# Kernel tuning notes

Measured on AMD Instinct MI355X. Metric: run time of the kernel, lower is better.

The kernel has to match this reference:

```python
import jax, jax.numpy as jnp
import numpy as np

N_HEADS = 2


def _ln(x, g, b, eps=1e-5):
    m = x.mean(-1, keepdims=True)
    v = ((x - m) ** 2).mean(-1, keepdims=True)
    return (x - m) * jax.lax.rsqrt(v + eps) * g + b


def _mha(x, in_w, in_b, out_w, out_b):
    # standard multi-head self-attention (relative/rotary branch is inert: query_pos=None)
    B, S, d = x.shape
    hd = d // N_HEADS
    qkv = x @ in_w.T + in_b
    q, k, v = jnp.split(qkv, 3, axis=-1)
    q = q.reshape(B, S, N_HEADS, hd)
    k = k.reshape(B, S, N_HEADS, hd)
    v = v.reshape(B, S, N_HEADS, hd)
    scores = jnp.einsum('bqhd,bkhd->bhqk', q, k) / jnp.sqrt(jnp.asarray(hd, x.dtype))
    attn = jax.nn.softmax(scores, axis=-1)
    o = jnp.einsum('bhqk,bkhd->bqhd', attn, v).reshape(B, S, d)
    return o @ out_w.T + out_b


def _forward(x, w1, b1, attn_in_w, attn_in_b, attn_out_w, attn_out_b, ln1_g, ln1_b,
             ffw_w1, ffw_b1, ffw_w2, ffw_b2, ln2_g, ln2_b,
             in_proj_w, conv_w, conv_b, x_proj_w, dt_proj_w, dt_proj_b, A_log, D, out_proj_w,
             w2a, b2a, w2b, b2b, w3a, b3a, w3b, b3b):
    # mlp1: (B,S,1) -> (B,S,d)
    h = x @ w1.T + b1
    # FFWRelativeSelfAttentionModule: 2 layers of post-norm MHA + FFW, take last output
    for i in range(2):
        a = _mha(h, attn_in_w[i], attn_in_b[i], attn_out_w[i], attn_out_b[i])
        h = _ln(h + a, ln1_g[i], ln1_b[i])
        f = jax.nn.relu(h @ ffw_w1[i].T + ffw_b1[i]) @ ffw_w2[i].T + ffw_b2[i]
        h = _ln(h + f, ln2_g[i], ln2_b[i])
    # Mamba block
    xz = h @ in_proj_w.T                       # (B,S,2*di)
    xm, z = jnp.split(xz, 2, axis=-1)          # (B,S,di) each
    S_len = xm.shape[1]
    dcv = conv_w.shape[1]
    xp = jnp.pad(xm, ((0, 0), (dcv - 1, 0), (0, 0)))   # causal depthwise conv1d
    xc = conv_b + sum(conv_w[:, k] * xp[:, k:k + S_len, :] for k in range(dcv))
    xc = jax.nn.silu(xc)
    xdb = xc @ x_proj_w.T                      # (B,S,dt_rank+2*N)
    dt_r = dt_proj_w.shape[1]
    N = A_log.shape[1]
    dti = xdb[..., :dt_r]
    Bm = xdb[..., dt_r:dt_r + N]
    Cm = xdb[..., dt_r + N:]
    dt = jax.nn.softplus(dti @ dt_proj_w.T + dt_proj_b)   # (B,S,di)
    A = -jnp.exp(A_log)                                    # (di,N)

    def step(hst, inp):
        dt_t, B_t, C_t, x_t = inp              # (B,di),(B,N),(B,N),(B,di)
        hst = hst * jnp.exp(dt_t[..., None] * A) + dt_t[..., None] * B_t[:, None, :] * x_t[..., None]
        y = jnp.einsum('bdn,bn->bd', hst, C_t)
        return hst, y

    h0 = jnp.zeros((xc.shape[0], A.shape[0], N), xc.dtype)
    xs = (jnp.swapaxes(dt, 0, 1), jnp.swapaxes(Bm, 0, 1),
          jnp.swapaxes(Cm, 0, 1), jnp.swapaxes(xc, 0, 1))
    _, ys = jax.lax.scan(step, h0, xs)
    y = jnp.swapaxes(ys, 0, 1) + D * xc
    y = y * jax.nn.silu(z)
    h = y @ out_proj_w.T                       # (B,S,d)
    # mlp2 (two stacked Linears, no activation) -> (B,S,1)
    o = (h @ w2a.T + b2a) @ w2b.T + b2b
    o = o.reshape(o.shape[0], -1)              # (B,9)
    # mlp3
    o = jax.nn.relu(o @ w3a.T + b3a) @ w3b.T + b3b
    return o


def setup_inputs() -> dict:
    key = jax.random.key(0)
    ks = jax.random.split(key, 16)
    d, N, dcv, di, dtr, B, S = 256, 16, 4, 512, 16, 4096, 9
    rn = lambda k, shp, s=0.02: jax.random.normal(k, shp, jnp.float32) * s
    return {
        'x': jax.random.normal(ks[0], (B, S, 1), jnp.float32),
        'w1': rn(ks[1], (d, 1), 0.5), 'b1': jnp.zeros((d,)),
        'attn_in_w': rn(ks[2], (2, 3 * d, d)), 'attn_in_b': jnp.zeros((2, 3 * d)),
        'attn_out_w': rn(ks[3], (2, d, d)), 'attn_out_b': jnp.zeros((2, d)),
        'ln1_g': jnp.ones((2, d)), 'ln1_b': jnp.zeros((2, d)),
        'ffw_w1': rn(ks[4], (2, d, d)), 'ffw_b1': jnp.zeros((2, d)),
        'ffw_w2': rn(ks[5], (2, d, d)), 'ffw_b2': jnp.zeros((2, d)),
        'ln2_g': jnp.ones((2, d)), 'ln2_b': jnp.zeros((2, d)),
        'in_proj_w': rn(ks[6], (2 * di, d)),
        'conv_w': rn(ks[7], (di, dcv), 0.2), 'conv_b': jnp.zeros((di,)),
        'x_proj_w': rn(ks[8], (dtr + 2 * N, di)),
        'dt_proj_w': rn(ks[9], (di, dtr), 0.1), 'dt_proj_b': jnp.full((di,), -4.0),
        'A_log': jnp.log(jnp.broadcast_to(jnp.arange(1, N + 1, dtype=jnp.float32), (di, N))),
        'D': jnp.ones((di,)),
        'out_proj_w': rn(ks[10], (d, di)),
        'w2a': rn(ks[11], (32, d)), 'b2a': jnp.zeros((32,)),
        'w2b': rn(ks[12], (1, 32)), 'b2b': jnp.zeros((1,)),
        'w3a': rn(ks[13], (9, 9), 0.3), 'b3a': jnp.zeros((9,)),
        'w3b': rn(ks[14], (1, 9), 0.3), 'b3b': jnp.zeros((1,)),
    }


def reference(x, w1, b1, attn_in_w, attn_in_b, attn_out_w, attn_out_b, ln1_g, ln1_b,
              ffw_w1, ffw_b1, ffw_w2, ffw_b2, ln2_g, ln2_b,
              in_proj_w, conv_w, conv_b, x_proj_w, dt_proj_w, dt_proj_b, A_log, D, out_proj_w,
              w2a, b2a, w2b, b2b, w3a, b3a, w3b, b3b):
    return _forward(x, w1, b1, attn_in_w, attn_in_b, attn_out_w, attn_out_b, ln1_g, ln1_b,
                    ffw_w1, ffw_b1, ffw_w2, ffw_b2, ln2_g, ln2_b,
                    in_proj_w, conv_w, conv_b, x_proj_w, dt_proj_w, dt_proj_b, A_log, D, out_proj_w,
                    w2a, b2a, w2b, b2b, w3a, b3a, w3b, b3b)
```

## Files before the change

### kernel.cpp

```cpp
#include <hip/hip_runtime.h>
#include <hip/hip_bf16.h>
#include <math.h>


#define BATCH 4096

typedef __attribute__((ext_vector_type(8))) short short8;
typedef __attribute__((ext_vector_type(4))) float f32x4;
typedef __attribute__((ext_vector_type(4))) unsigned short u16x4;
typedef unsigned short ushort;

__device__ __forceinline__ ushort f2bf(float f) {
    unsigned u = __float_as_uint(f);
    u += 0x7fffu + ((u >> 16) & 1u);
    return (ushort)(u >> 16);
}
__device__ __forceinline__ float bf2f(ushort u) {
    return __uint_as_float(((unsigned)u) << 16);
}

__global__ __launch_bounds__(256) void convw_kernel(
    const float* __restrict__ s0, const float* __restrict__ s1,
    const float* __restrict__ s2, const float* __restrict__ s3,
    const float* __restrict__ s4, const float* __restrict__ s5,
    ushort* __restrict__ dst)
{
    int i = blockIdx.x * 256 + threadIdx.x;
    float v;
    if      (i < 393216)  v = s0[i];
    else if (i < 524288)  v = s1[i - 393216];
    else if (i < 655360)  v = s2[i - 524288];
    else if (i < 786432)  v = s3[i - 655360];
    else if (i < 1048576) v = s4[i - 786432];
    else                  v = s5[i - 1048576];
    dst[i] = f2bf(v);
}

__global__ __launch_bounds__(256) void embed_kernel(
    const float* __restrict__ x, const float* __restrict__ w1,
    const float* __restrict__ b1, float* __restrict__ h,
    ushort* __restrict__ hbf, int r0, int nr)
{
    int i = blockIdx.x * 256 + threadIdx.x;
    if (i >= nr * 256) return;
    int c  = i & 255;
    int row = i >> 8;
    float v = x[r0 + row] * w1[c] + b1[c];
    h[i] = v;
    hbf[i] = f2bf(v);
}

__global__ __launch_bounds__(256) void mgemm_kernel(
    const ushort* __restrict__ A, const ushort* __restrict__ W,
    const float* __restrict__ bias, float* __restrict__ Cf,
    ushort* __restrict__ Cb, const float* __restrict__ yin,
    int M, int N, int K, int lda, int act, int outmode)
{
    __shared__ ushort As[128 * 64];
    __shared__ ushort Bs[128 * 64];

    const int tid  = threadIdx.x;
    const int m0   = blockIdx.x * 128;
    const int n0   = blockIdx.y * 128;
    const int wid  = tid >> 6, lane = tid & 63;
    const int wr   = wid >> 1, wc = wid & 1;
    const int lrow = lane & 15, lk8 = lane >> 4, l7 = lane & 7;
    const int trow = tid >> 3, tchk = tid & 7;

    f32x4 acc[4][4];
    #pragma unroll
    for (int i = 0; i < 4; ++i)
        #pragma unroll
        for (int j = 0; j < 4; ++j)
            acc[i][j] = f32x4{0.f, 0.f, 0.f, 0.f};

    for (int k0 = 0; k0 < K; k0 += 64) {
        #pragma unroll
        for (int p = 0; p < 4; ++p) {
            const int r = p * 32 + trow;
            const short8 av = *reinterpret_cast<const short8*>(
                &A[(size_t)(m0 + r) * lda + k0 + tchk * 8]);
            const short8 wv = *reinterpret_cast<const short8*>(
                &W[(size_t)(n0 + r) * K + k0 + tchk * 8]);
            const int off = r * 64 + ((tchk ^ (r & 7)) << 3);
            *reinterpret_cast<short8*>(&As[off]) = av;
            *reinterpret_cast<short8*>(&Bs[off]) = wv;
        }
        __syncthreads();

        #pragma unroll
        for (int kh = 0; kh < 2; ++kh) {
            short8 af[4], bf[4];
            #pragma unroll
            for (int i = 0; i < 4; ++i) {
                const int ra = wr * 64 + i * 16 + lrow;
                const int rb = wc * 64 + i * 16 + lrow;
                const int sl = ((kh << 2) | lk8) ^ l7;
                af[i] = *reinterpret_cast<const short8*>(&As[ra * 64 + sl * 8]);
                bf[i] = *reinterpret_cast<const short8*>(&Bs[rb * 64 + sl * 8]);
            }
            #pragma unroll
            for (int i = 0; i < 4; ++i)
                #pragma unroll
                for (int j = 0; j < 4; ++j)
                    acc[i][j] = __builtin_amdgcn_mfma_f32_16x16x32_bf16(
                        af[i], bf[j], acc[i][j], 0, 0, 0);
        }
        __syncthreads();
    }

    const int cb = n0 + wc * 64 + lrow;
    const int rb = m0 + wr * 64 + lk8 * 4;
    float bj[4];
    #pragma unroll
    for (int j = 0; j < 4; ++j) bj[j] = bias ? bias[cb + j * 16] : 0.f;

    #pragma unroll
    for (int i = 0; i < 4; ++i) {
        #pragma unroll
        for (int r = 0; r < 4; ++r) {
            const size_t mrow = (size_t)(rb + i * 16 + r) * N;
            #pragma unroll
            for (int j = 0; j < 4; ++j) {
                float v = acc[i][j][r] + bj[j];
                const size_t idx = mrow + cb + j * 16;
                if (act == 1) v = fmaxf(v, 0.f);
                if (outmode == 0) {
                    Cf[idx] = v;
                } else if (outmode == 1) {
                    Cb[idx] = f2bf(v);
                } else {
                    const float sig = 1.f / (1.f + __expf(-v));
                    Cb[idx] = f2bf(yin[idx] * (v * sig));
                }
            }
        }
    }
}

__global__ __launch_bounds__(256) void sgemm_kernel(
    const float* __restrict__ A, const float* __restrict__ W,
    const float* __restrict__ bias, float* __restrict__ C,
    int M, int N, int K, int lda, int act)
{
    __shared__ float As[16][68];
    __shared__ float Ws[16][68];
    const int tid = threadIdx.x;
    const int m0 = blockIdx.y * 64;
    const int n0 = blockIdx.x * 64;
    const int tm = tid >> 4;
    const int tn = tid & 15;
    const int lrow = tid >> 2;
    const int lk   = (tid & 3) * 4;

    float acc[4][4] = {};

    for (int k0 = 0; k0 < K; k0 += 16) {
        {
            int m = m0 + lrow;
            float4 v = make_float4(0.f, 0.f, 0.f, 0.f);
            if (m < M) v = *reinterpret_cast<const float4*>(&A[(size_t)m * lda + k0 + lk]);
            As[lk + 0][lrow] = v.x; As[lk + 1][lrow] = v.y;
            As[lk + 2][lrow] = v.z; As[lk + 3][lrow] = v.w;
            int n = n0 + lrow;
            float4 w = make_float4(0.f, 0.f, 0.f, 0.f);
            if (n < N) w = *reinterpret_cast<const float4*>(&W[(size_t)n * K + k0 + lk]);
            Ws[lk + 0][lrow] = w.x; Ws[lk + 1][lrow] = w.y;
            Ws[lk + 2][lrow] = w.z; Ws[lk + 3][lrow] = w.w;
        }
        __syncthreads();
        #pragma unroll
        for (int k = 0; k < 16; ++k) {
            float4 av = *reinterpret_cast<const float4*>(&As[k][tm * 4]);
            float4 wv = *reinterpret_cast<const float4*>(&Ws[k][tn * 4]);
            float a[4] = {av.x, av.y, av.z, av.w};
            float w[4] = {wv.x, wv.y, wv.z, wv.w};
            #pragma unroll
            for (int i = 0; i < 4; ++i)
                #pragma unroll
                for (int j = 0; j < 4; ++j)
                    acc[i][j] = fmaf(a[i], w[j], acc[i][j]);
        }
        __syncthreads();
    }

    #pragma unroll
    for (int i = 0; i < 4; ++i) {
        int m = m0 + tm * 4 + i;
        if (m >= M) continue;
        #pragma unroll
        for (int j = 0; j < 4; ++j) {
            int n = n0 + tn * 4 + j;
            if (n >= N) continue;
            float v = acc[i][j];
            if (bias) v += bias[n];
            if (act == 1) v = fmaxf(v, 0.f);
            C[(size_t)m * N + n] = v;
        }
    }
}

__global__ __launch_bounds__(128) void attn_kernel(
    const ushort* __restrict__ qkv, ushort* __restrict__ o, int nb)
{
    __shared__ float q[9][132], kk[9][132], v[9][132];
    __shared__ float sc[9][12];
    const int blk = blockIdx.x;
    if (blk >= nb * 2) return;
    const int b = blk >> 1, head = blk & 1;
    const int t = threadIdx.x;
    const size_t base = (size_t)b * 9 * 768 + (size_t)head * 128;
    #pragma unroll
    for (int s = 0; s < 9; ++s) {
        q[s][t]  = bf2f(qkv[base + s * 768 + t]);
        kk[s][t] = bf2f(qkv[base + s * 768 + 256 + t]);
        v[s][t]  = bf2f(qkv[base + s * 768 + 512 + t]);
    }
    __syncthreads();
    if (t < 81) {
        int qi = t / 9, ki = t % 9;
        float acc = 0.f;
        #pragma unroll 8
        for (int c = 0; c < 128; ++c) acc = fmaf(q[qi][c], kk[ki][c], acc);
        sc[qi][ki] = acc * 0.08838834764831845f;
    }
    __syncthreads();
    if (t < 9) {
        float mx = -1e30f;
        #pragma unroll
        for (int k2 = 0; k2 < 9; ++k2) mx = fmaxf(mx, sc[t][k2]);
        float e[9], sum = 0.f;
        #pragma unroll
        for (int k2 = 0; k2 < 9; ++k2) { e[k2] = __expf(sc[t][k2] - mx); sum += e[k2]; }
        float inv = 1.f / sum;
        #pragma unroll
        for (int k2 = 0; k2 < 9; ++k2) sc[t][k2] = e[k2] * inv;
    }
    __syncthreads();
    #pragma unroll
    for (int qi = 0; qi < 9; ++qi) {
        float acc = 0.f;
        #pragma unroll
        for (int k2 = 0; k2 < 9; ++k2) acc = fmaf(sc[qi][k2], v[k2][t], acc);
        o[(size_t)(b * 9 + qi) * 256 + head * 128 + t] = f2bf(acc);
    }
}

__global__ __launch_bounds__(256) void ln_add_kernel(
    const float* __restrict__ h, const float* __restrict__ a,
    const float* __restrict__ g, const float* __restrict__ bb,
    float* __restrict__ out, ushort* __restrict__ outbf, int nrows)
{
    const int wave = threadIdx.x >> 6;
    const int lane = threadIdx.x & 63;
    const int row = blockIdx.x * 4 + wave;
    if (row >= nrows) return;
    const float4 hv = reinterpret_cast<const float4*>(h + (size_t)row * 256)[lane];
    const float4 av = reinterpret_cast<const float4*>(a + (size_t)row * 256)[lane];
    float x0 = hv.x + av.x, x1 = hv.y + av.y, x2 = hv.z + av.z, x3 = hv.w + av.w;
    float s  = x0 + x1 + x2 + x3;
    float sq = x0 * x0 + x1 * x1 + x2 * x2 + x3 * x3;
    #pragma unroll
    for (int off = 32; off; off >>= 1) {
        s  += __shfl_down(s, off);
        sq += __shfl_down(sq, off);
    }
    s = __shfl(s, 0); sq = __shfl(sq, 0);
    const float mean = s * (1.f / 256.f);
    const float var  = sq * (1.f / 256.f) - mean * mean;
    const float inv  = rsqrtf(var + 1e-5f);
    const float4 gv = reinterpret_cast<const float4*>(g)[lane];
    const float4 bv = reinterpret_cast<const float4*>(bb)[lane];
    float4 ov;
    ov.x = (x0 - mean) * inv * gv.x + bv.x;
    ov.y = (x1 - mean) * inv * gv.y + bv.y;
    ov.z = (x2 - mean) * inv * gv.z + bv.z;
    ov.w = (x3 - mean) * inv * gv.w + bv.w;
    reinterpret_cast<float4*>(out + (size_t)row * 256)[lane] = ov;
    u16x4 bf;
    bf.x = f2bf(ov.x); bf.y = f2bf(ov.y); bf.z = f2bf(ov.z); bf.w = f2bf(ov.w);
    reinterpret_cast<u16x4*>(outbf + (size_t)row * 256)[lane] = bf;
}

__global__ __launch_bounds__(256) void conv_silu2_kernel(
    const float* __restrict__ xm, const float* __restrict__ cw,
    const float* __restrict__ cb, float* __restrict__ xc, int nb)
{
    int i = blockIdx.x * 256 + threadIdx.x;
    if (i >= nb * 512) return;
    const int c = i & 511, b = i >> 9;
    float xmv[9];
    #pragma unroll
    for (int s = 0; s < 9; ++s)
        xmv[s] = xm[(size_t)(b * 9 + s) * 512 + c];
    const float4 cwv4 = *reinterpret_cast<const float4*>(&cw[c * 4]);
    const float cwv[4] = {cwv4.x, cwv4.y, cwv4.z, cwv4.w};
    const float cbv = cb[c];
    #pragma unroll
    for (int s = 0; s < 9; ++s) {
        float acc = cbv;
        #pragma unroll
        for (int k = 0; k < 4; ++k) {
            const int sp = s + k - 3;
            if (sp >= 0) acc = fmaf(cwv[k], xmv[sp], acc);
        }
        const float sig = 1.f / (1.f + __expf(-acc));
        xc[(size_t)(b * 9 + s) * 512 + c] = acc * sig;
    }
}

__global__ __launch_bounds__(512) void scan_kernel(
    float* __restrict__ xcy, const float* __restrict__ xdb,
    const float* __restrict__ dt_w, const float* __restrict__ dt_b,
    const float* __restrict__ A_log, const float* __restrict__ Dp)
{
    __shared__ float sx[9 * 48];
    const int c = threadIdx.x;
    const int b = blockIdx.x;
    if (c < 108) {
        reinterpret_cast<float4*>(sx)[c] =
            reinterpret_cast<const float4*>(xdb + (size_t)b * 432)[c];
    }

    float wdt[16], Ar[16];
    #pragma unroll
    for (int n = 0; n < 16; n += 4) {
        const float4 wv4 = *reinterpret_cast<const float4*>(&dt_w[c * 16 + n]);
        wdt[n] = wv4.x; wdt[n + 1] = wv4.y; wdt[n + 2] = wv4.z; wdt[n + 3] = wv4.w;
        const float4 av4 = *reinterpret_cast<const float4*>(&A_log[c * 16 + n]);
        Ar[n] = -__expf(av4.x); Ar[n + 1] = -__expf(av4.y);
        Ar[n + 2] = -__expf(av4.z); Ar[n + 3] = -__expf(av4.w);
    }
    const float dtb = dt_b[c];
    const float Dc  = Dp[c];
    const float a1  = Ar[0];
    bool chain = true;
    #pragma unroll
    for (int n = 1; n < 16; ++n)
        chain = chain && (fabsf(Ar[n] - (float)(n + 1) * a1) <=
                          1e-3f * (float)(n + 1) * fabsf(a1));
    __syncthreads();

    float hst[16] = {};
    for (int s = 0; s < 9; ++s) {
        const float* xb = sx + s * 48;
        float dti = dtb;
        #pragma unroll
        for (int n = 0; n < 16; ++n) dti = fmaf(xb[n], wdt[n], dti);
        const float dt = (dti > 20.f) ? dti : __logf(1.f + __expf(dti));
        const size_t idx = (size_t)(b * 9 + s) * 512 + c;
        const float xv = xcy[idx];
        const float dtx = dt * xv;
        float acc = 0.f;
        if (chain) {
            const float e1 = __expf(dt * a1);
            float en = 1.f;
            #pragma unroll
            for (int n = 0; n < 16; ++n) {
                en *= e1;
                hst[n] = fmaf(hst[n], en, dtx * xb[16 + n]);
                acc = fmaf(hst[n], xb[32 + n], acc);
            }
        } else {
            #pragma unroll
            for (int n = 0; n < 16; ++n) {
                hst[n] = fmaf(hst[n], __expf(dt * Ar[n]), dtx * xb[16 + n]);
                acc = fmaf(hst[n], xb[32 + n], acc);
            }
        }
        xcy[idx] = acc + Dc * xv;
    }
}

__global__ __launch_bounds__(256) void head_kernel(
    const float* __restrict__ t32, const float* __restrict__ w2b,
    const float* __restrict__ b2b, const float* __restrict__ w3a,
    const float* __restrict__ b3a, const float* __restrict__ w3b,
    const float* __restrict__ b3b, float* __restrict__ out, int b0, int nb)
{
    int b = blockIdx.x * 256 + threadIdx.x;
    if (b >= nb) return;
    float o9[9];
    #pragma unroll
    for (int s = 0; s < 9; ++s) {
        const float* r = t32 + (size_t)(b * 9 + s) * 32;
        float acc = b2b[0];
        #pragma unroll
        for (int k = 0; k < 32; ++k) acc = fmaf(r[k], w2b[k], acc);
        o9[s] = acc;
    }
    float accout = b3b[0];
    #pragma unroll
    for (int j = 0; j < 9; ++j) {
        float rj = b3a[j];
        #pragma unroll
        for (int s = 0; s < 9; ++s) rj = fmaf(o9[s], w3a[j * 9 + s], rj);
        rj = fmaxf(rj, 0.f);
        accout = fmaf(rj, w3b[j], accout);
    }
    out[b0 + b] = accout;
}

extern "C" void kernel_launch(void* const* d_in, const int* in_sizes, int n_in,
                              void* d_out, int out_size, void* d_ws, size_t ws_size,
                              hipStream_t stream)
{
    const float* x          = (const float*)d_in[0];
    const float* w1         = (const float*)d_in[1];
    const float* b1         = (const float*)d_in[2];
    const float* attn_in_w  = (const float*)d_in[3];
    const float* attn_in_b  = (const float*)d_in[4];
    const float* attn_out_w = (const float*)d_in[5];
    const float* attn_out_b = (const float*)d_in[6];
    const float* ln1_g      = (const float*)d_in[7];
    const float* ln1_b      = (const float*)d_in[8];
    const float* ffw_w1     = (const float*)d_in[9];
    const float* ffw_b1     = (const float*)d_in[10];
    const float* ffw_w2     = (const float*)d_in[11];
    const float* ffw_b2     = (const float*)d_in[12];
    const float* ln2_g      = (const float*)d_in[13];
    const float* ln2_b      = (const float*)d_in[14];
    const float* in_proj_w  = (const float*)d_in[15];
    const float* conv_w     = (const float*)d_in[16];
    const float* conv_b     = (const float*)d_in[17];
    const float* x_proj_w   = (const float*)d_in[18];
    const float* dt_proj_w  = (const float*)d_in[19];
    const float* dt_proj_b  = (const float*)d_in[20];
    const float* A_log      = (const float*)d_in[21];
    const float* Dp         = (const float*)d_in[22];
    const float* out_proj_w = (const float*)d_in[23];
    const float* w2a        = (const float*)d_in[24];
    const float* b2a        = (const float*)d_in[25];
    const float* w2b        = (const float*)d_in[26];
    const float* b2b        = (const float*)d_in[27];
    const float* w3a        = (const float*)d_in[28];
    const float* b3a        = (const float*)d_in[29];
    const float* w3b        = (const float*)d_in[30];
    const float* b3b        = (const float*)d_in[31];
    float* out = (float*)d_out;

    const size_t WB_FLOATS = 589824;
    const size_t PER_ROW = 1792;
    int nchunks = 1;
    while (nchunks < 32 &&
           (WB_FLOATS + (size_t)(BATCH / nchunks) * 9 * PER_ROW) * sizeof(float) > ws_size)
        nchunks <<= 1;
    const int nb = BATCH / nchunks;
    const int nr = nb * 9;
    const size_t CAPR = (size_t)nr;

    ushort* WB = (ushort*)d_ws;
    float*  AR = (float*)d_ws + WB_FLOATS;

    ushort* wb_attn_in  = WB;
    ushort* wb_attn_out = WB + 393216;
    ushort* wb_ffw1     = WB + 524288;
    ushort* wb_ffw2     = WB + 655360;
    ushort* wb_inproj_x = WB + 786432;
    ushort* wb_inproj_z = WB + 917504;
    ushort* wb_outproj  = WB + 1048576;

    hipLaunchKernelGGL(convw_kernel, dim3(1179648 / 256), dim3(256), 0, stream,
                       attn_in_w, attn_out_w, ffw_w1, ffw_w2, in_proj_w,
                       out_proj_w, WB);

    auto gemm = [&](const float* A, const float* W, const float* bias, float* C,
                    int M, int N, int K, int lda, int act) {
        dim3 grid((N + 63) / 64, (M + 63) / 64);
        hipLaunchKernelGGL(sgemm_kernel, grid, dim3(256), 0, stream,
                           A, W, bias, C, M, N, K, lda, act);
    };
    auto mgemm = [&](const ushort* A, const ushort* W, const float* bias,
                     float* Cf, ushort* Cb, const float* yin,
                     int M, int N, int K, int lda, int act, int outmode) {
        dim3 grid(M / 128, N / 128);
        hipLaunchKernelGGL(mgemm_kernel, grid, dim3(256), 0, stream,
                           A, W, bias, Cf, Cb, yin, M, N, K, lda, act, outmode);
    };

    for (int ck = 0; ck < nchunks; ++ck) {
        const int b0 = ck * nb;
        const int r0 = b0 * 9;

        float*  h    = AR;
        ushort* hbf  = (ushort*)(AR + CAPR * 256);
        float*  aux  = AR + CAPR * 384;
        ushort* aobf = (ushort*)aux;
        float*  big  = AR + CAPR * 512;
        ushort* qkvb = (ushort*)big;
        float*  aa   = big;
        ushort* f1bf = (ushort*)(big + CAPR * 256);
        float*  f2   = big + CAPR * 384;
        float*  xm   = big;
        ushort* ybf  = (ushort*)(big + CAPR * 512);
        float*  xc   = AR + CAPR * 1280;
        float*  xdb  = aux;
        float*  h2   = h;
        float*  t32  = aux;

        hipLaunchKernelGGL(embed_kernel, dim3((nr * 256 + 255) / 256), dim3(256),
                           0, stream, x, w1, b1, h, hbf, r0, nr);

        for (int i = 0; i < 2; ++i) {
            mgemm(hbf, wb_attn_in + (size_t)i * 196608, attn_in_b + i * 768,
                  nullptr, qkvb, nullptr, nr, 768, 256, 256, 0, 1);
            hipLaunchKernelGGL(attn_kernel, dim3(nb * 2), dim3(128), 0, stream,
                               qkvb, aobf, nb);
            mgemm(aobf, wb_attn_out + (size_t)i * 65536, attn_out_b + i * 256,
                  aa, nullptr, nullptr, nr, 256, 256, 256, 0, 0);
            hipLaunchKernelGGL(ln_add_kernel, dim3((nr + 3) / 4), dim3(256), 0, stream,
                               h, aa, ln1_g + i * 256, ln1_b + i * 256, h, hbf, nr);
            mgemm(hbf, wb_ffw1 + (size_t)i * 65536, ffw_b1 + i * 256,
                  nullptr, f1bf, nullptr, nr, 256, 256, 256, 1, 1);
            mgemm(f1bf, wb_ffw2 + (size_t)i * 65536, ffw_b2 + i * 256,
                  f2, nullptr, nullptr, nr, 256, 256, 256, 0, 0);
            hipLaunchKernelGGL(ln_add_kernel, dim3((nr + 3) / 4), dim3(256), 0, stream,
                               h, f2, ln2_g + i * 256, ln2_b + i * 256, h, hbf, nr);
        }

        mgemm(hbf, wb_inproj_x, nullptr, xm, nullptr, nullptr,
              nr, 512, 256, 256, 0, 0);
        hipLaunchKernelGGL(conv_silu2_kernel, dim3((nb * 512 + 255) / 256), dim3(256),
                           0, stream, xm, conv_w, conv_b, xc, nb);
        gemm(xc, x_proj_w, nullptr, xdb, nr, 48, 512, 512, 0);
        hipLaunchKernelGGL(scan_kernel, dim3(nb), dim3(512), 0, stream,
                           xc, xdb, dt_proj_w, dt_proj_b, A_log, Dp);
        mgemm(hbf, wb_inproj_z, nullptr, nullptr, ybf, xc,
              nr, 512, 256, 256, 0, 2);
        mgemm(ybf, wb_outproj, nullptr, h2, nullptr, nullptr,
              nr, 256, 512, 512, 0, 0);
        gemm(h2, w2a, b2a, t32, nr, 32, 256, 256, 0);
        hipLaunchKernelGGL(head_kernel, dim3((nb + 255) / 256), dim3(256), 0, stream,
                           t32, w2b, b2b, w3a, b3a, w3b, b3b, out, b0, nb);
    }
}
```

Baseline: 743.3 us.

## Load GEMM tiles straight to LDS and shorten exp power chain in scan

The GEMM tile loads now use global_load_lds, which writes 16-byte chunks directly into shared memory and skips the register round trip. The XOR swizzle moves to the global source address, so each wave writes 8 contiguous rows. Separately, the chained-A scan path builds the powers e^(n*dt*a1) with a tree of products rather than a serial multiply chain, which cuts the dependency depth. The direct-to-LDS path depends on the builtin's per-lane layout matching the swizzled reads, and the loop still has no double buffering.

```diff
diff --git a/kernel.cpp b/kernel.cpp
--- a/kernel.cpp
+++ b/kernel.cpp
@@ -9,6 +9,10 @@
 typedef __attribute__((ext_vector_type(4))) float f32x4;
 typedef __attribute__((ext_vector_type(4))) unsigned short u16x4;
 typedef unsigned short ushort;
+
+#define GLD16(gp, lp) __builtin_amdgcn_global_load_lds( \
+    (const __attribute__((address_space(1))) unsigned int*)(gp), \
+    (__attribute__((address_space(3))) unsigned int*)(lp), 16, 0, 0)
 
 __device__ __forceinline__ ushort f2bf(float f) {
     unsigned u = __float_as_uint(f);
@@ -65,7 +69,7 @@
     const int wid  = tid >> 6, lane = tid & 63;
     const int wr   = wid >> 1, wc = wid & 1;
     const int lrow = lane & 15, lk8 = lane >> 4, l7 = lane & 7;
-    const int trow = tid >> 3, tchk = tid & 7;
+    const int rw   = lane >> 3, sl8 = lane & 7;
 
     f32x4 acc[4][4];
     #pragma unroll
@@ -75,16 +79,13 @@
             acc[i][j] = f32x4{0.f, 0.f, 0.f, 0.f};
 
     for (int k0 = 0; k0 < K; k0 += 64) {
+        const int ka = (sl8 ^ rw) * 8;
         #pragma unroll
         for (int p = 0; p < 4; ++p) {
-            const int r = p * 32 + trow;
-            const short8 av = *reinterpret_cast<const short8*>(
-                &A[(size_t)(m0 + r) * lda + k0 + tchk * 8]);
-            const short8 wv = *reinterpret_cast<const short8*>(
-                &W[(size_t)(n0 + r) * K + k0 + tchk * 8]);
-            const int off = r * 64 + ((tchk ^ (r & 7)) << 3);
-            *reinterpret_cast<short8*>(&As[off]) = av;
-            *reinterpret_cast<short8*>(&Bs[off]) = wv;
+            const int r0 = (p * 4 + wid) * 8;
+            const int r  = r0 + rw;
+            GLD16(&A[(size_t)(m0 + r) * lda + k0 + ka], &As[r0 * 64]);
+            GLD16(&W[(size_t)(n0 + r) * K   + k0 + ka], &Bs[r0 * 64]);
         }
         __syncthreads();
 
@@ -353,12 +354,16 @@
         const float dtx = dt * xv;
         float acc = 0.f;
         if (chain) {
-            const float e1 = __expf(dt * a1);
-            float en = 1.f;
+            float e[16];
+            e[0] = __expf(dt * a1);
+            #pragma unroll
+            for (int n = 1; n < 16; ++n) {
+                const int a = (n - 1) >> 1;
+                e[n] = e[a] * e[n - 1 - a];
+            }
             #pragma unroll
             for (int n = 0; n < 16; ++n) {
-                en *= e1;
-                hst[n] = fmaf(hst[n], en, dtx * xb[16 + n]);
+                hst[n] = fmaf(hst[n], e[n], dtx * xb[16 + n]);
                 acc = fmaf(hst[n], xb[32 + n], acc);
             }
         } else {
```

New measurement: 739.5 us. No clear change (-0.5%).
